# Performance work log

Hardware: AMD Instinct MI355X
Metric: run time of the kernel (lower is better)

The kernel has to match this reference:

```python
import jax, jax.numpy as jnp
import numpy as np
import math

B, T, D_MODEL, N_HEAD = 2, 2048, 1024, 16
NUM_BUCKETS, MAX_DIST = 32, 128
D_HEAD = D_MODEL // N_HEAD


def _relative_position_bucket(rel_pos, num_buckets=NUM_BUCKETS, max_distance=MAX_DIST):
    # bidirectional=True branch of the torch code
    nb = num_buckets // 2
    buckets = (rel_pos > 0).astype(jnp.int32) * nb
    rel_pos = jnp.abs(rel_pos)
    max_exact = nb // 2
    is_small = rel_pos < max_exact
    # guard log(0); masked out by is_small anyway
    large = max_exact + (
        jnp.log(jnp.maximum(rel_pos, 1).astype(jnp.float32) / max_exact)
        / math.log(max_distance / max_exact) * (nb - max_exact)
    ).astype(jnp.int32)
    large = jnp.minimum(large, nb - 1)
    return buckets + jnp.where(is_small, rel_pos, large)


def compute_bias(rel_bias, q_len, kv_len):
    qp = jnp.arange(q_len, dtype=jnp.int32)[:, None]
    kp = jnp.arange(kv_len, dtype=jnp.int32)[None, :]
    buckets = _relative_position_bucket(kp - qp)          # [Tq, Tkv]
    vals = rel_bias[buckets]                              # [Tq, Tkv, H]
    return jnp.transpose(vals, (2, 0, 1))                 # [H, Tq, Tkv]


def setup_inputs() -> dict:
    key = jax.random.key(0)
    ks = jax.random.split(key, 9)
    inp = {
        'q': jax.random.normal(ks[0], (B, T, D_MODEL), jnp.float32),
        'k': jax.random.normal(ks[1], (B, T, D_MODEL), jnp.float32),
        'v': jax.random.normal(ks[2], (B, T, D_MODEL), jnp.float32),
        'mask': jax.random.randint(ks[3], (B, T, T), 0, 2, jnp.int32),
        'Wq': jax.random.normal(ks[4], (D_MODEL, D_MODEL), jnp.float32) * 0.02,
        'Wk': jax.random.normal(ks[5], (D_MODEL, D_MODEL), jnp.float32) * 0.02,
        'Wv': jax.random.normal(ks[6], (D_MODEL, D_MODEL), jnp.float32) * 0.02,
        'Wfc': jax.random.normal(ks[7], (D_MODEL, D_MODEL), jnp.float32) * 0.02,
        'rel_bias': jax.random.normal(ks[8], (NUM_BUCKETS, N_HEAD), jnp.float32) * 0.02,
    }
    return inp


def reference(q, k, v, mask, Wq, Wk, Wv, Wfc, rel_bias):
    b, tq, _ = q.shape
    tkv = k.shape[1]
    qh = (q @ Wq).reshape(b, tq, N_HEAD, D_HEAD)
    kh = (k @ Wk).reshape(b, tkv, N_HEAD, D_HEAD)
    vh = (v @ Wv).reshape(b, tkv, N_HEAD, D_HEAD)
    attn = jnp.einsum('blhd,bthd->bhlt', qh, kh) / np.sqrt(D_HEAD).astype(np.float32)
    position_bias = compute_bias(rel_bias, tq, tkv)       # [H, Tq, Tkv]
    attn = attn + position_bias[None]                     # broadcast over batch
    attn = jnp.where(mask[:, None] == 0, -1e9, attn)
    attn = jax.nn.softmax(attn, axis=-1)                  # dropout: eval mode (identity)
    out = jnp.einsum('bhlt,bthd->blhd', attn, vh).reshape(b, tq, D_MODEL)
    out = out @ Wfc
    return out, position_bias[:, None]                    # bias returned as [H,1,Tq,Tkv] like torch
```

## Files before the change

### kernel.cpp

```cpp
#include <hip/hip_runtime.h>
#include <math.h>

#define TT 2048
#define BB 2
#define HH 16
#define DMODEL 1024
#define NREL 4095

typedef __attribute__((ext_vector_type(8)))  _Float16 half8;
typedef __attribute__((ext_vector_type(4)))  _Float16 half4;
typedef __attribute__((ext_vector_type(16))) float    f32x16;
typedef __attribute__((ext_vector_type(4)))  int      int4v;

__device__ __forceinline__ f32x16 zero16() {
    f32x16 v;
#pragma unroll
    for (int i = 0; i < 16; ++i) v[i] = 0.f;
    return v;
}

__device__ __forceinline__ unsigned pkh(float a, float b) {
    union { _Float16 h[2]; unsigned u; } x;
    x.h[0] = (_Float16)a; x.h[1] = (_Float16)b;
    return x.u;
}

__device__ __forceinline__ void gload16(const void* g, void* l) {
    __builtin_amdgcn_global_load_lds(
        (const __attribute__((address_space(1))) void*)g,
        (__attribute__((address_space(3))) void*)l, 16, 0, 0);
}

__device__ __forceinline__ int rel_bucket(int rel) {
    int base = rel > 0 ? 16 : 0;
    int r = rel < 0 ? -rel : rel;
    int lb;
    if (r < 8)       lb = r;
    else if (r < 12) lb = 8;
    else if (r < 16) lb = 9;
    else if (r < 23) lb = 10;
    else if (r < 32) lb = 11;
    else if (r < 46) lb = 12;
    else if (r < 64) lb = 13;
    else if (r < 91) lb = 14;
    else             lb = 15;
    return base + lb;
}

__global__ __launch_bounds__(256) void prep_kernel(
    const float* __restrict__ q, const float* __restrict__ k,
    const float* __restrict__ v, const int* __restrict__ mask,
    const float* __restrict__ W0, const float* __restrict__ W1,
    const float* __restrict__ W2, const float* __restrict__ W3,
    const float* __restrict__ rel_bias,
    _Float16* __restrict__ q16, _Float16* __restrict__ k16,
    _Float16* __restrict__ v16, _Float16* __restrict__ WT,
    float* __restrict__ btable, unsigned* __restrict__ mb)
{
    __shared__ float t[64][65];
    int bid = blockIdx.x, tid = threadIdx.x;
    if (bid < 256) {
        int idx = bid * 256 + tid;
        if (idx < HH * NREL) {
            int h = idx / NREL, ri = idx % NREL;
            btable[idx] = rel_bias[rel_bucket(ri - (TT - 1)) * HH + h];
        }
    } else if (bid < 1280) {
        int zz = (bid - 256) >> 8, inner = (bid - 256) & 255;
        const float* src = zz == 0 ? W0 : zz == 1 ? W1 : zz == 2 ? W2 : W3;
        _Float16* dst = WT + (size_t)zz * DMODEL * DMODEL;
        int k0 = (inner >> 4) * 64, n0 = (inner & 15) * 64;
        int r = tid >> 4, c4 = (tid & 15) * 4;
#pragma unroll
        for (int i = 0; i < 4; ++i) {
            float4 vv = *(const float4*)(src + (size_t)(k0 + r + 16 * i) * DMODEL + n0 + c4);
            t[r + 16 * i][c4] = vv.x; t[r + 16 * i][c4 + 1] = vv.y;
            t[r + 16 * i][c4 + 2] = vv.z; t[r + 16 * i][c4 + 3] = vv.w;
        }
        __syncthreads();
        int rn = tid >> 2, ck = (tid & 3) * 16;
        half8 h0, h1;
#pragma unroll
        for (int j = 0; j < 8; ++j) h0[j] = (_Float16)t[ck + j][rn];
#pragma unroll
        for (int j = 0; j < 8; ++j) h1[j] = (_Float16)t[ck + 8 + j][rn];
        *(half8*)(dst + (size_t)(n0 + rn) * DMODEL + k0 + ck) = h0;
        *(half8*)(dst + (size_t)(n0 + rn) * DMODEL + k0 + ck + 8) = h1;
    } else if (bid < 7424) {
        int zz = (bid - 1280) >> 11, inner = (bid - 1280) & 2047;
        const float* src = zz == 0 ? q : zz == 1 ? k : v;
        _Float16* dst = zz == 0 ? q16 : zz == 1 ? k16 : v16;
        int i = inner * 256 + tid;
        const float4* in4 = (const float4*)src;
        float4 v0 = in4[(size_t)i * 2], v1 = in4[(size_t)i * 2 + 1];
        half8 h = {(_Float16)v0.x, (_Float16)v0.y, (_Float16)v0.z, (_Float16)v0.w,
                   (_Float16)v1.x, (_Float16)v1.y, (_Float16)v1.z, (_Float16)v1.w};
        *(half8*)(dst + (size_t)i * 8) = h;
    } else {
        int g = (bid - 7424) * 256 + tid;
        int vv = mask[g];
        unsigned long long bal = __ballot(vv != 0);
        if ((g & 63) == 0) {
            int word = g >> 5;
            mb[word]     = (unsigned)bal;
            mb[word + 1] = (unsigned)(bal >> 32);
        }
    }
}

__global__ __launch_bounds__(256) void gemm_proj3(
    const _Float16* __restrict__ q16, const _Float16* __restrict__ k16,
    const _Float16* __restrict__ v16, const _Float16* __restrict__ WT,
    _Float16* __restrict__ qhf, _Float16* __restrict__ khf,
    _Float16* __restrict__ vtf, int zbase)
{
    __shared__ __align__(16) char lds[65536];
    int z = zbase + blockIdx.z;
    const _Float16* A  = z == 0 ? q16 : z == 1 ? k16 : v16;
    const _Float16* Bt = WT + (size_t)z * DMODEL * DMODEL;
    int bm = blockIdx.x * 128, bn = blockIdx.y * 128;
    int tid = threadIdx.x;
    int wv = tid >> 6, lane = tid & 63, hi = lane >> 5;
    int lo = lane & 31;
    int wr = wv >> 1, wc = wv & 1;
    int srow = wv * 32 + (lane >> 3);
    int scol = (lane & 7) * 8;
    const _Float16* Abase = A  + (size_t)(bm + srow) * DMODEL + scol;
    const _Float16* Bbase = Bt + (size_t)(bn + srow) * DMODEL + scol;

    f32x16 acc[2][2];
    acc[0][0] = zero16(); acc[0][1] = zero16();
    acc[1][0] = zero16(); acc[1][1] = zero16();

    auto stage = [&](int buf, int kt) {
#pragma unroll
        for (int t = 0; t < 4; ++t) {
            gload16(Abase + (size_t)t * 8 * DMODEL + kt * 64, lds + buf + wv * 4096 + t * 1024);
            gload16(Bbase + (size_t)t * 8 * DMODEL + kt * 64, lds + buf + 16384 + wv * 4096 + t * 1024);
        }
    };
    auto compute = [&](int buf) {
#pragma unroll
        for (int kk = 0; kk < 4; ++kk) {
            int cs = 2 * kk + hi;
            half8 a[2], b[2];
#pragma unroll
            for (int i = 0; i < 2; ++i) {
                a[i] = *(const half8*)(lds + buf + (wr * 64 + i * 32 + lo) * 128 + cs * 16);
                b[i] = *(const half8*)(lds + buf + 16384 + (wc * 64 + i * 32 + lo) * 128 + cs * 16);
            }
            acc[0][0] = __builtin_amdgcn_mfma_f32_32x32x16_f16(a[0], b[0], acc[0][0], 0, 0, 0);
            acc[0][1] = __builtin_amdgcn_mfma_f32_32x32x16_f16(a[0], b[1], acc[0][1], 0, 0, 0);
            acc[1][0] = __builtin_amdgcn_mfma_f32_32x32x16_f16(a[1], b[0], acc[1][0], 0, 0, 0);
            acc[1][1] = __builtin_amdgcn_mfma_f32_32x32x16_f16(a[1], b[1], acc[1][1], 0, 0, 0);
        }
    };

    stage(0, 0);
    __syncthreads();
    for (int kt = 0; kt < 16; kt += 2) {
        stage(32768, kt + 1);
        compute(0);
        __syncthreads();
        stage(0, kt + 2 < 16 ? kt + 2 : 15);
        compute(32768);
        __syncthreads();
    }

    if (z < 2) {
        _Float16* C = z == 0 ? qhf : khf;
#pragma unroll
        for (int j = 0; j < 2; ++j) {
            int n = bn + wc * 64 + j * 32 + lo;
            int h = n >> 6, d = n & 63;
#pragma unroll
            for (int i = 0; i < 2; ++i) {
                int mb2 = bm + wr * 64 + i * 32 + 4 * hi;
#pragma unroll
                for (int r = 0; r < 16; ++r) {
                    int m = mb2 + (r & 3) + 8 * (r >> 2);
                    int b = m >> 11, t = m & (TT - 1);
                    C[((size_t)(b * HH + h) * TT + t) * 64 + d] = (_Float16)acc[i][j][r];
                }
            }
        }
    } else {
#pragma unroll
        for (int j = 0; j < 2; ++j) {
            int n = bn + wc * 64 + j * 32 + lo;
            int h = n >> 6, d = n & 63;
#pragma unroll
            for (int i = 0; i < 2; ++i) {
                int mb2 = bm + wr * 64 + i * 32 + 4 * hi;
                int b = mb2 >> 11, tb = mb2 & (TT - 1);
#pragma unroll
                for (int r4 = 0; r4 < 4; ++r4) {
                    half4 hv = {(_Float16)acc[i][j][4 * r4 + 0], (_Float16)acc[i][j][4 * r4 + 1],
                                (_Float16)acc[i][j][4 * r4 + 2], (_Float16)acc[i][j][4 * r4 + 3]};
                    *(half4*)(vtf + ((size_t)(b * HH + h) * 64 + d) * TT + tb + 8 * r4) = hv;
                }
            }
        }
    }
}

template<int NSPLIT>
__global__ __launch_bounds__(256, 2) void attn_mfma(
    const _Float16* __restrict__ qh, const _Float16* __restrict__ kh,
    const _Float16* __restrict__ vt, const unsigned* __restrict__ maskbits,
    const float* __restrict__ btable, _Float16* __restrict__ Oout,
    float* __restrict__ ml)
{
    __shared__ float bias_lds[4096];
    int bid = blockIdx.x;
    int j = bid >> 3;
    int qt = j & 15;
    int sp, grp;
    if (NSPLIT == 2) { sp = (j >> 4) & 1; grp = j >> 5; }
    else             { sp = 0;            grp = j >> 4; }
    int bh = (bid & 7) + 8 * grp;
    int h = bh & 15, b = bh >> 4;
    int tid = threadIdx.x;
    int wv = tid >> 6, lane = tid & 63, lo = lane & 31, hi = lane >> 5;
    int q0 = qt * 128 + wv * 32;

    {
        const float* bsrc = btable + h * NREL;
#pragma unroll
        for (int i = 0; i < 16; ++i) {
            int idx = i * 256 + tid;
            bias_lds[idx] = bsrc[idx < NREL ? idx : NREL - 1];
        }
    }

    const size_t bhoff = (size_t)(b * HH + h);
    const _Float16* Q = qh + (bhoff * TT + q0) * 64;
    const _Float16* K = kh + bhoff * TT * 64;
    const _Float16* V = vt + bhoff * 64 * TT;

    half8 qf[4];
#pragma unroll
    for (int c = 0; c < 4; ++c)
        qf[c] = *(const half8*)(Q + (size_t)lo * 64 + c * 16 + hi * 8);

    const int bofs = (TT - 1) - (q0 + lo) + 4 * hi;
    const unsigned* mw = maskbits + ((size_t)b * TT + q0 + lo) * 64;

    f32x16 acco0 = zero16(), acco1 = zero16();
    float m = -INFINITY, l = 0.f;

    __syncthreads();

    const int ktb = sp * (32 / NSPLIT);
    for (int kt = ktb; kt < ktb + 32 / NSPLIT; ++kt) {
        int k0 = kt * 64;
        unsigned wm0 = mw[2 * kt], wm1 = mw[2 * kt + 1];

        f32x16 accs0 = zero16(), accs1 = zero16();
        {
            half8 kf[4];
#pragma unroll
            for (int c = 0; c < 4; ++c)
                kf[c] = *(const half8*)(K + (size_t)(k0 + lo) * 64 + c * 16 + hi * 8);
            __builtin_amdgcn_s_setprio(1);
#pragma unroll
            for (int c = 0; c < 4; ++c)
                accs0 = __builtin_amdgcn_mfma_f32_32x32x16_f16(kf[c], qf[c], accs0, 0, 0, 0);
            __builtin_amdgcn_s_setprio(0);
#pragma unroll
            for (int c = 0; c < 4; ++c)
                kf[c] = *(const half8*)(K + (size_t)(k0 + 32 + lo) * 64 + c * 16 + hi * 8);
            __builtin_amdgcn_s_setprio(1);
#pragma unroll
            for (int c = 0; c < 4; ++c)
                accs1 = __builtin_amdgcn_mfma_f32_32x32x16_f16(kf[c], qf[c], accs1, 0, 0, 0);
            __builtin_amdgcn_s_setprio(0);
        }

        unsigned ws0 = wm0 >> (hi * 4), ws1 = wm1 >> (hi * 4);
        int bbase = bofs + k0;
#pragma unroll
        for (int r = 0; r < 16; ++r) {
            int sh = (r & 3) + 8 * (r >> 2);
            float s0 = fmaf(accs0[r], 0.125f, bias_lds[bbase + sh]);
            float s1 = fmaf(accs1[r], 0.125f, bias_lds[bbase + sh + 32]);
            accs0[r] = ((ws0 >> sh) & 1) ? s0 : -1e9f;
            accs1[r] = ((ws1 >> sh) & 1) ? s1 : -1e9f;
        }

        float tr[8];
#pragma unroll
        for (int r = 0; r < 8; ++r)
            tr[r] = fmaxf(fmaxf(accs0[r], accs0[r + 8]), fmaxf(accs1[r], accs1[r + 8]));
#pragma unroll
        for (int r = 0; r < 4; ++r) tr[r] = fmaxf(tr[r], tr[r + 4]);
        float tm = fmaxf(fmaxf(tr[0], tr[1]), fmaxf(tr[2], tr[3]));
        tm = fmaxf(tm, __shfl_xor(tm, 32));
        float mnew = fmaxf(m, tm);
        float corr = __expf(m - mnew);
        m = mnew;

#pragma unroll
        for (int r = 0; r < 16; ++r) accs0[r] = __expf(accs0[r] - m);
#pragma unroll
        for (int r = 0; r < 16; ++r) accs1[r] = __expf(accs1[r] - m);
#pragma unroll
        for (int r = 0; r < 8; ++r)
            tr[r] = (accs0[r] + accs0[r + 8]) + (accs1[r] + accs1[r + 8]);
#pragma unroll
        for (int r = 0; r < 4; ++r) tr[r] += tr[r + 4];
        float rs = (tr[0] + tr[1]) + (tr[2] + tr[3]);
        rs += __shfl_xor(rs, 32);
        l = l * corr + rs;
#pragma unroll
        for (int r = 0; r < 16; ++r) { acco0[r] *= corr; acco1[r] *= corr; }

        half8 pb[4];
#pragma unroll
        for (int g = 0; g < 2; ++g)
#pragma unroll
            for (int hc = 0; hc < 2; ++hc) {
                int r0 = hc * 8;
                float p0 = g ? accs1[r0 + 0] : accs0[r0 + 0];
                float p1 = g ? accs1[r0 + 1] : accs0[r0 + 1];
                float p2 = g ? accs1[r0 + 2] : accs0[r0 + 2];
                float p3 = g ? accs1[r0 + 3] : accs0[r0 + 3];
                float p4 = g ? accs1[r0 + 4] : accs0[r0 + 4];
                float p5 = g ? accs1[r0 + 5] : accs0[r0 + 5];
                float p6 = g ? accs1[r0 + 6] : accs0[r0 + 6];
                float p7 = g ? accs1[r0 + 7] : accs0[r0 + 7];
                unsigned w0 = pkh(p0, p1);
                unsigned w2 = pkh(p4, p5);
                asm("v_permlane32_swap_b32 %0, %1" : "+v"(w0), "+v"(w2));
                unsigned w1 = pkh(p2, p3);
                unsigned w3 = pkh(p6, p7);
                asm("v_permlane32_swap_b32 %0, %1" : "+v"(w1), "+v"(w3));
                union { int4v i; half8 hf; } cv;
                cv.i = (int4v){(int)w0, (int)w1, (int)w2, (int)w3};
                pb[2 * g + hc] = cv.hf;
            }

        {
            half8 vf[4];
#pragma unroll
            for (int c = 0; c < 4; ++c)
                vf[c] = *(const half8*)(V + (size_t)lo * TT + k0 + c * 16 + hi * 8);
            __builtin_amdgcn_s_setprio(1);
#pragma unroll
            for (int c = 0; c < 4; ++c)
                acco0 = __builtin_amdgcn_mfma_f32_32x32x16_f16(vf[c], pb[c], acco0, 0, 0, 0);
            __builtin_amdgcn_s_setprio(0);
#pragma unroll
            for (int c = 0; c < 4; ++c)
                vf[c] = *(const half8*)(V + (size_t)(32 + lo) * TT + k0 + c * 16 + hi * 8);
            __builtin_amdgcn_s_setprio(1);
#pragma unroll
            for (int c = 0; c < 4; ++c)
                acco1 = __builtin_amdgcn_mfma_f32_32x32x16_f16(vf[c], pb[c], acco1, 0, 0, 0);
            __builtin_amdgcn_s_setprio(0);
        }
    }

    float inv = 1.f / l;
    _Float16* op = Oout + (size_t)sp * (BB * HH * TT * 64) + (bhoff * TT + q0 + lo) * 64;
#pragma unroll
    for (int r4 = 0; r4 < 4; ++r4) {
        int d0 = 8 * r4 + 4 * hi;
        half4 h0 = {(_Float16)(acco0[4 * r4 + 0] * inv), (_Float16)(acco0[4 * r4 + 1] * inv),
                    (_Float16)(acco0[4 * r4 + 2] * inv), (_Float16)(acco0[4 * r4 + 3] * inv)};
        *(half4*)(op + d0) = h0;
        half4 h1 = {(_Float16)(acco1[4 * r4 + 0] * inv), (_Float16)(acco1[4 * r4 + 1] * inv),
                    (_Float16)(acco1[4 * r4 + 2] * inv), (_Float16)(acco1[4 * r4 + 3] * inv)};
        *(half4*)(op + d0 + 32) = h1;
    }
    if (NSPLIT == 2 && hi == 0) {
        int row = (int)(bhoff * TT) + q0 + lo;
        ml[sp * 131072 + row]         = m;
        ml[sp * 131072 + 65536 + row] = l;
    }
}

__global__ __launch_bounds__(256) void combine_kernel(
    const _Float16* __restrict__ Ohalf, const float* __restrict__ ml,
    _Float16* __restrict__ O)
{
    int idx = blockIdx.x * 256 + threadIdx.x;
    int row = idx >> 3, d8 = (idx & 7) * 8;
    float m0 = ml[row],          l0 = ml[65536 + row];
    float m1 = ml[131072 + row], l1 = ml[196608 + row];
    float mm = fmaxf(m0, m1);
    float w0 = __expf(m0 - mm) * l0, w1 = __expf(m1 - mm) * l1;
    float dn = fmaxf(w0 + w1, 1e-30f);
    float c0 = w0 / dn, c1 = w1 / dn;
    half8 a = *(const half8*)(Ohalf + (size_t)row * 64 + d8);
    half8 b = *(const half8*)(Ohalf + (size_t)(BB * HH * TT * 64) + (size_t)row * 64 + d8);
    half8 o;
#pragma unroll
    for (int jj = 0; jj < 8; ++jj)
        o[jj] = (_Float16)(c0 * (float)a[jj] + c1 * (float)b[jj]);
    *(half8*)(O + (size_t)row * 64 + d8) = o;
}

__global__ __launch_bounds__(256) void fc_bias_kernel(
    const _Float16* __restrict__ O, const _Float16* __restrict__ Bt,
    float* __restrict__ out0, const float* __restrict__ btable,
    float* __restrict__ out1)
{
    __shared__ __align__(16) char lds[65536];
    int bid = blockIdx.x, tid = threadIdx.x;
    if (bid >= 256) {
        const int n4 = HH * TT * TT / 4, stride = 2048 * 256;
        for (int i4 = (bid - 256) * 256 + tid; i4 < n4; i4 += stride) {
            int i = i4 * 4;
            int kk = i & (TT - 1);
            int qq = (i >> 11) & (TT - 1);
            int hh2 = i >> 22;
            const float* btp = btable + hh2 * NREL + (kk - qq + (TT - 1));
            float4 vv = make_float4(btp[0], btp[1], btp[2], btp[3]);
            reinterpret_cast<float4*>(out1)[i4] = vv;
        }
        return;
    }
    int bm = (bid & 31) * 128, bn = (bid >> 5) * 128;
    int wv = tid >> 6, lane = tid & 63, lo = lane & 31, hi = lane >> 5;
    int wr = wv >> 1, wc = wv & 1;
    int srow = wv * 32 + (lane >> 3);
    int scol = (lane & 7) * 8;
    int bb = bm >> 11, tbase = bm & (TT - 1);
    const _Float16* Abase = O + ((size_t)(bb * HH) * TT + tbase + srow) * 64 + scol;
    const _Float16* Bbase = Bt + (size_t)(bn + srow) * DMODEL + scol;

    f32x16 acc[2][2];
    acc[0][0] = zero16(); acc[0][1] = zero16();
    acc[1][0] = zero16(); acc[1][1] = zero16();

    auto stage = [&](int buf, int kt) {
#pragma unroll
        for (int t = 0; t < 4; ++t) {
            gload16(Abase + (size_t)kt * TT * 64 + (size_t)t * 8 * 64, lds + buf + wv * 4096 + t * 1024);
            gload16(Bbase + (size_t)t * 8 * DMODEL + kt * 64, lds + buf + 16384 + wv * 4096 + t * 1024);
        }
    };
    auto compute = [&](int buf) {
#pragma unroll
        for (int kk = 0; kk < 4; ++kk) {
            int cs = 2 * kk + hi;
            half8 a[2], b[2];
#pragma unroll
            for (int i = 0; i < 2; ++i) {
                a[i] = *(const half8*)(lds + buf + (wr * 64 + i * 32 + lo) * 128 + cs * 16);
                b[i] = *(const half8*)(lds + buf + 16384 + (wc * 64 + i * 32 + lo) * 128 + cs * 16);
            }
            acc[0][0] = __builtin_amdgcn_mfma_f32_32x32x16_f16(a[0], b[0], acc[0][0], 0, 0, 0);
            acc[0][1] = __builtin_amdgcn_mfma_f32_32x32x16_f16(a[0], b[1], acc[0][1], 0, 0, 0);
            acc[1][0] = __builtin_amdgcn_mfma_f32_32x32x16_f16(a[1], b[0], acc[1][0], 0, 0, 0);
            acc[1][1] = __builtin_amdgcn_mfma_f32_32x32x16_f16(a[1], b[1], acc[1][1], 0, 0, 0);
        }
    };

    stage(0, 0);
    __syncthreads();
    for (int kt = 0; kt < 16; kt += 2) {
        stage(32768, kt + 1);
        compute(0);
        __syncthreads();
        stage(0, kt + 2 < 16 ? kt + 2 : 15);
        compute(32768);
        __syncthreads();
    }

#pragma unroll
    for (int j = 0; j < 2; ++j) {
        int n = bn + wc * 64 + j * 32 + lo;
#pragma unroll
        for (int i = 0; i < 2; ++i) {
            int mb2 = bm + wr * 64 + i * 32 + 4 * hi;
#pragma unroll
            for (int r = 0; r < 16; ++r) {
                int m = mb2 + (r & 3) + 8 * (r >> 2);
                out0[(size_t)m * DMODEL + n] = acc[i][j][r];
            }
        }
    }
}

extern "C" void kernel_launch(void* const* d_in, const int* in_sizes, int n_in,
                              void* d_out, int out_size, void* d_ws, size_t ws_size,
                              hipStream_t stream) {
    const float* q        = (const float*)d_in[0];
    const float* k        = (const float*)d_in[1];
    const float* v        = (const float*)d_in[2];
    const int*   mask     = (const int*)  d_in[3];
    const float* Wq       = (const float*)d_in[4];
    const float* Wk       = (const float*)d_in[5];
    const float* Wv       = (const float*)d_in[6];
    const float* Wfc      = (const float*)d_in[7];
    const float* rel_bias = (const float*)d_in[8];

    float* out0 = (float*)d_out;
    float* out1 = out0 + (size_t)BB * TT * DMODEL;

    char* w = (char*)d_ws;
    _Float16* q16 = (_Float16*)(w);
    _Float16* k16 = (_Float16*)(w + ((size_t)8  << 20));
    _Float16* v16 = (_Float16*)(w + ((size_t)16 << 20));
    _Float16* qhf = (_Float16*)(w + ((size_t)24 << 20));
    _Float16* khf = (_Float16*)(w + ((size_t)32 << 20));
    _Float16* WT  = (_Float16*)(w + ((size_t)40 << 20));
    float*    btable = (float*)(w + ((size_t)48 << 20));
    unsigned* mbits  = (unsigned*)(w + ((size_t)48 << 20) + ((size_t)1 << 19));
    bool big = ws_size >= ((size_t)58 << 20);
    _Float16* vtf = big ? (_Float16*)(w + ((size_t)49 << 20) + ((size_t)1 << 19))
                        : k16;
    _Float16* Ohalf = (_Float16*)w;
    float*    ml    = (float*)(w + ((size_t)40 << 20));
    _Float16* O     = v16;

    prep_kernel<<<dim3(40192), dim3(256), 0, stream>>>(
        q, k, v, mask, Wq, Wk, Wv, Wfc, rel_bias, q16, k16, v16, WT, btable, mbits);

    if (big) {
        gemm_proj3<<<dim3(32, 8, 3), dim3(256), 0, stream>>>(q16, k16, v16, WT,
                                                             qhf, khf, vtf, 0);
        attn_mfma<2><<<dim3(BB * HH * 16 * 2), dim3(256), 0, stream>>>(
            qhf, khf, vtf, mbits, btable, Ohalf, ml);
        combine_kernel<<<dim3(2048), dim3(256), 0, stream>>>(Ohalf, ml, O);
    } else {
        gemm_proj3<<<dim3(32, 8, 1), dim3(256), 0, stream>>>(q16, k16, v16, WT, qhf, khf, vtf, 0);
        gemm_proj3<<<dim3(32, 8, 1), dim3(256), 0, stream>>>(q16, k16, v16, WT, qhf, khf, vtf, 1);
        gemm_proj3<<<dim3(32, 8, 1), dim3(256), 0, stream>>>(q16, k16, v16, WT, qhf, khf, vtf, 2);
        attn_mfma<1><<<dim3(BB * HH * 16), dim3(256), 0, stream>>>(
            qhf, khf, vtf, mbits, btable, O, ml);
    }

    fc_bias_kernel<<<dim3(2304), dim3(256), 0, stream>>>(
        O, WT + (size_t)3 * DMODEL * DMODEL, out0, btable, out1);
}
```

Baseline: 293.6 us.

## Drop split-KV attention, process 128-key tiles, and use exp2 softmax

```diff
diff --git a/kernel.cpp b/kernel.cpp
--- a/kernel.cpp
+++ b/kernel.cpp
@@ -11,6 +11,8 @@
 typedef __attribute__((ext_vector_type(4)))  _Float16 half4;
 typedef __attribute__((ext_vector_type(16))) float    f32x16;
 typedef __attribute__((ext_vector_type(4)))  int      int4v;
+
+#define EXP2F(x) __builtin_amdgcn_exp2f(x)
 
 __device__ __forceinline__ f32x16 zero16() {
     f32x16 v;
@@ -204,21 +206,15 @@
     }
 }
 
-template<int NSPLIT>
-__global__ __launch_bounds__(256, 2) void attn_mfma(
+__global__ __launch_bounds__(256) void attn_mfma(
     const _Float16* __restrict__ qh, const _Float16* __restrict__ kh,
     const _Float16* __restrict__ vt, const unsigned* __restrict__ maskbits,
-    const float* __restrict__ btable, _Float16* __restrict__ Oout,
-    float* __restrict__ ml)
+    const float* __restrict__ btable, _Float16* __restrict__ Oout)
 {
     __shared__ float bias_lds[4096];
     int bid = blockIdx.x;
-    int j = bid >> 3;
-    int qt = j & 15;
-    int sp, grp;
-    if (NSPLIT == 2) { sp = (j >> 4) & 1; grp = j >> 5; }
-    else             { sp = 0;            grp = j >> 4; }
-    int bh = (bid & 7) + 8 * grp;
+    int xcd = bid & 7, j = bid >> 3;
+    int qt = j & 15, bh = xcd + 8 * (j >> 4);
     int h = bh & 15, b = bh >> 4;
     int tid = threadIdx.x;
     int wv = tid >> 6, lane = tid & 63, lo = lane & 31, hi = lane >> 5;
@@ -229,7 +225,7 @@
 #pragma unroll
         for (int i = 0; i < 16; ++i) {
             int idx = i * 256 + tid;
-            bias_lds[idx] = bsrc[idx < NREL ? idx : NREL - 1];
+            bias_lds[idx] = bsrc[idx < NREL ? idx : NREL - 1] * 1.44269504f;
         }
     }
 
@@ -245,18 +241,19 @@
 
     const int bofs = (TT - 1) - (q0 + lo) + 4 * hi;
     const unsigned* mw = maskbits + ((size_t)b * TT + q0 + lo) * 64;
+    const float SC = 0.125f * 1.44269504f;
 
     f32x16 acco0 = zero16(), acco1 = zero16();
     float m = -INFINITY, l = 0.f;
 
     __syncthreads();
 
-    const int ktb = sp * (32 / NSPLIT);
-    for (int kt = ktb; kt < ktb + 32 / NSPLIT; ++kt) {
-        int k0 = kt * 64;
-        unsigned wm0 = mw[2 * kt], wm1 = mw[2 * kt + 1];
-
-        f32x16 accs0 = zero16(), accs1 = zero16();
+    for (int kt = 0; kt < 16; ++kt) {
+        int k0 = kt * 128;
+        unsigned wmA0 = mw[4 * kt], wmA1 = mw[4 * kt + 1];
+        unsigned wmB0 = mw[4 * kt + 2], wmB1 = mw[4 * kt + 3];
+
+        f32x16 sA0 = zero16(), sA1 = zero16(), sB0 = zero16(), sB1 = zero16();
         {
             half8 kf[4];
 #pragma unroll
@@ -265,7 +262,7 @@
             __builtin_amdgcn_s_setprio(1);
 #pragma unroll
             for (int c = 0; c < 4; ++c)
-                accs0 = __builtin_amdgcn_mfma_f32_32x32x16_f16(kf[c], qf[c], accs0, 0, 0, 0);
+                sA0 = __builtin_amdgcn_mfma_f32_32x32x16_f16(kf[c], qf[c], sA0, 0, 0, 0);
             __builtin_amdgcn_s_setprio(0);
 #pragma unroll
             for (int c = 0; c < 4; ++c)
@@ -273,40 +270,69 @@
             __builtin_amdgcn_s_setprio(1);
 #pragma unroll
             for (int c = 0; c < 4; ++c)
-                accs1 = __builtin_amdgcn_mfma_f32_32x32x16_f16(kf[c], qf[c], accs1, 0, 0, 0);
-            __builtin_amdgcn_s_setprio(0);
-        }
-
-        unsigned ws0 = wm0 >> (hi * 4), ws1 = wm1 >> (hi * 4);
+                sA1 = __builtin_amdgcn_mfma_f32_32x32x16_f16(kf[c], qf[c], sA1, 0, 0, 0);
+            __builtin_amdgcn_s_setprio(0);
+#pragma unroll
+            for (int c = 0; c < 4; ++c)
+                kf[c] = *(const half8*)(K + (size_t)(k0 + 64 + lo) * 64 + c * 16 + hi * 8);
+            __builtin_amdgcn_s_setprio(1);
+#pragma unroll
+            for (int c = 0; c < 4; ++c)
+                sB0 = __builtin_amdgcn_mfma_f32_32x32x16_f16(kf[c], qf[c], sB0, 0, 0, 0);
+            __builtin_amdgcn_s_setprio(0);
+#pragma unroll
+            for (int c = 0; c < 4; ++c)
+                kf[c] = *(const half8*)(K + (size_t)(k0 + 96 + lo) * 64 + c * 16 + hi * 8);
+            __builtin_amdgcn_s_setprio(1);
+#pragma unroll
+            for (int c = 0; c < 4; ++c)
+                sB1 = __builtin_amdgcn_mfma_f32_32x32x16_f16(kf[c], qf[c], sB1, 0, 0, 0);
+            __builtin_amdgcn_s_setprio(0);
+        }
+
+        unsigned wsA0 = wmA0 >> (hi * 4), wsA1 = wmA1 >> (hi * 4);
+        unsigned wsB0 = wmB0 >> (hi * 4), wsB1 = wmB1 >> (hi * 4);
         int bbase = bofs + k0;
 #pragma unroll
         for (int r = 0; r < 16; ++r) {
             int sh = (r & 3) + 8 * (r >> 2);
-            float s0 = fmaf(accs0[r], 0.125f, bias_lds[bbase + sh]);
-            float s1 = fmaf(accs1[r], 0.125f, bias_lds[bbase + sh + 32]);
-            accs0[r] = ((ws0 >> sh) & 1) ? s0 : -1e9f;
-            accs1[r] = ((ws1 >> sh) & 1) ? s1 : -1e9f;
+            float a0 = fmaf(sA0[r], SC, bias_lds[bbase + sh]);
+            float a1 = fmaf(sA1[r], SC, bias_lds[bbase + sh + 32]);
+            float b0 = fmaf(sB0[r], SC, bias_lds[bbase + sh + 64]);
+            float b1 = fmaf(sB1[r], SC, bias_lds[bbase + sh + 96]);
+            sA0[r] = ((wsA0 >> sh) & 1) ? a0 : -1e9f;
+            sA1[r] = ((wsA1 >> sh) & 1) ? a1 : -1e9f;
+            sB0[r] = ((wsB0 >> sh) & 1) ? b0 : -1e9f;
+            sB1[r] = ((wsB1 >> sh) & 1) ? b1 : -1e9f;
         }
 
         float tr[8];
 #pragma unroll
-        for (int r = 0; r < 8; ++r)
-            tr[r] = fmaxf(fmaxf(accs0[r], accs0[r + 8]), fmaxf(accs1[r], accs1[r + 8]));
+        for (int r = 0; r < 8; ++r) {
+            float x0 = fmaxf(fmaxf(sA0[r], sA0[r + 8]), fmaxf(sA1[r], sA1[r + 8]));
+            float x1 = fmaxf(fmaxf(sB0[r], sB0[r + 8]), fmaxf(sB1[r], sB1[r + 8]));
+            tr[r] = fmaxf(x0, x1);
+        }
 #pragma unroll
         for (int r = 0; r < 4; ++r) tr[r] = fmaxf(tr[r], tr[r + 4]);
         float tm = fmaxf(fmaxf(tr[0], tr[1]), fmaxf(tr[2], tr[3]));
         tm = fmaxf(tm, __shfl_xor(tm, 32));
         float mnew = fmaxf(m, tm);
-        float corr = __expf(m - mnew);
+        float corr = EXP2F(m - mnew);
         m = mnew;
 
 #pragma unroll
-        for (int r = 0; r < 16; ++r) accs0[r] = __expf(accs0[r] - m);
-#pragma unroll
-        for (int r = 0; r < 16; ++r) accs1[r] = __expf(accs1[r] - m);
+        for (int r = 0; r < 16; ++r) sA0[r] = EXP2F(sA0[r] - m);
+#pragma unroll
+        for (int r = 0; r < 16; ++r) sA1[r] = EXP2F(sA1[r] - m);
+#pragma unroll
+        for (int r = 0; r < 16; ++r) sB0[r] = EXP2F(sB0[r] - m);
+#pragma unroll
+        for (int r = 0; r < 16; ++r) sB1[r] = EXP2F(sB1[r] - m);
 #pragma unroll
         for (int r = 0; r < 8; ++r)
-            tr[r] = (accs0[r] + accs0[r + 8]) + (accs1[r] + accs1[r + 8]);
+            tr[r] = ((sA0[r] + sA0[r + 8]) + (sA1[r] + sA1[r + 8]))
+                  + ((sB0[r] + sB0[r + 8]) + (sB1[r] + sB1[r + 8]));
 #pragma unroll
         for (int r = 0; r < 4; ++r) tr[r] += tr[r + 4];
         float rs = (tr[0] + tr[1]) + (tr[2] + tr[3]);
@@ -315,20 +341,20 @@
 #pragma unroll
         for (int r = 0; r < 16; ++r) { acco0[r] *= corr; acco1[r] *= corr; }
 
-        half8 pb[4];
+        half8 pbA[4], pbB[4];
 #pragma unroll
         for (int g = 0; g < 2; ++g)
 #pragma unroll
             for (int hc = 0; hc < 2; ++hc) {
                 int r0 = hc * 8;
-                float p0 = g ? accs1[r0 + 0] : accs0[r0 + 0];
-                float p1 = g ? accs1[r0 + 1] : accs0[r0 + 1];
-                float p2 = g ? accs1[r0 + 2] : accs0[r0 + 2];
-                float p3 = g ? accs1[r0 + 3] : accs0[r0 + 3];
-                float p4 = g ? accs1[r0 + 4] : accs0[r0 + 4];
-                float p5 = g ? accs1[r0 + 5] : accs0[r0 + 5];
-                float p6 = g ? accs1[r0 + 6] : accs0[r0 + 6];
-                float p7 = g ? accs1[r0 + 7] : accs0[r0 + 7];
+                float p0 = g ? sA1[r0 + 0] : sA0[r0 + 0];
+                float p1 = g ? sA1[r0 + 1] : sA0[r0 + 1];
+                float p2 = g ? sA1[r0 + 2] : sA0[r0 + 2];
+                float p3 = g ? sA1[r0 + 3] : sA0[r0 + 3];
+                float p4 = g ? sA1[r0 + 4] : sA0[r0 + 4];
+                float p5 = g ? sA1[r0 + 5] : sA0[r0 + 5];
+                float p6 = g ? sA1[r0 + 6] : sA0[r0 + 6];
+                float p7 = g ? sA1[r0 + 7] : sA0[r0 + 7];
                 unsigned w0 = pkh(p0, p1);
                 unsigned w2 = pkh(p4, p5);
                 asm("v_permlane32_swap_b32 %0, %1" : "+v"(w0), "+v"(w2));
@@ -337,7 +363,30 @@
                 asm("v_permlane32_swap_b32 %0, %1" : "+v"(w1), "+v"(w3));
                 union { int4v i; half8 hf; } cv;
                 cv.i = (int4v){(int)w0, (int)w1, (int)w2, (int)w3};
-                pb[2 * g + hc] = cv.hf;
+                pbA[2 * g + hc] = cv.hf;
+            }
+#pragma unroll
+        for (int g = 0; g < 2; ++g)
+#pragma unroll
+            for (int hc = 0; hc < 2; ++hc) {
+                int r0 = hc * 8;
+                float p0 = g ? sB1[r0 + 0] : sB0[r0 + 0];
+                float p1 = g ? sB1[r0 + 1] : sB0[r0 + 1];
+                float p2 = g ? sB1[r0 + 2] : sB0[r0 + 2];
+                float p3 = g ? sB1[r0 + 3] : sB0[r0 + 3];
+                float p4 = g ? sB1[r0 + 4] : sB0[r0 + 4];
+                float p5 = g ? sB1[r0 + 5] : sB0[r0 + 5];
+                float p6 = g ? sB1[r0 + 6] : sB0[r0 + 6];
+                float p7 = g ? sB1[r0 + 7] : sB0[r0 + 7];
+                unsigned w0 = pkh(p0, p1);
+                unsigned w2 = pkh(p4, p5);
+                asm("v_permlane32_swap_b32 %0, %1" : "+v"(w0), "+v"(w2));
+                unsigned w1 = pkh(p2, p3);
+                unsigned w3 = pkh(p6, p7);
+                asm("v_permlane32_swap_b32 %0, %1" : "+v"(w1), "+v"(w3));
+                union { int4v i; half8 hf; } cv;
+                cv.i = (int4v){(int)w0, (int)w1, (int)w2, (int)w3};
+                pbB[2 * g + hc] = cv.hf;
             }
 
         {
@@ -348,7 +397,15 @@
             __builtin_amdgcn_s_setprio(1);
 #pragma unroll
             for (int c = 0; c < 4; ++c)
-                acco0 = __builtin_amdgcn_mfma_f32_32x32x16_f16(vf[c], pb[c], acco0, 0, 0, 0);
+                acco0 = __builtin_amdgcn_mfma_f32_32x32x16_f16(vf[c], pbA[c], acco0, 0, 0, 0);
+            __builtin_amdgcn_s_setprio(0);
+#pragma unroll
+            for (int c = 0; c < 4; ++c)
+                vf[c] = *(const half8*)(V + (size_t)lo * TT + k0 + 64 + c * 16 + hi * 8);
+            __builtin_amdgcn_s_setprio(1);
+#pragma unroll
+            for (int c = 0; c < 4; ++c)
+                acco0 = __builtin_amdgcn_mfma_f32_32x32x16_f16(vf[c], pbB[c], acco0, 0, 0, 0);
             __builtin_amdgcn_s_setprio(0);
 #pragma unroll
             for (int c = 0; c < 4; ++c)
@@ -356,13 +413,21 @@
             __builtin_amdgcn_s_setprio(1);
 #pragma unroll
             for (int c = 0; c < 4; ++c)
-                acco1 = __builtin_amdgcn_mfma_f32_32x32x16_f16(vf[c], pb[c], acco1, 0, 0, 0);
+                acco1 = __builtin_amdgcn_mfma_f32_32x32x16_f16(vf[c], pbA[c], acco1, 0, 0, 0);
+            __builtin_amdgcn_s_setprio(0);
+#pragma unroll
+            for (int c = 0; c < 4; ++c)
+                vf[c] = *(const half8*)(V + (size_t)(32 + lo) * TT + k0 + 64 + c * 16 + hi * 8);
+            __builtin_amdgcn_s_setprio(1);
+#pragma unroll
+            for (int c = 0; c < 4; ++c)
+                acco1 = __builtin_amdgcn_mfma_f32_32x32x16_f16(vf[c], pbB[c], acco1, 0, 0, 0);
             __builtin_amdgcn_s_setprio(0);
         }
     }
 
     float inv = 1.f / l;
-    _Float16* op = Oout + (size_t)sp * (BB * HH * TT * 64) + (bhoff * TT + q0 + lo) * 64;
+    _Float16* op = Oout + (bhoff * TT + q0 + lo) * 64;
 #pragma unroll
     for (int r4 = 0; r4 < 4; ++r4) {
         int d0 = 8 * r4 + 4 * hi;
@@ -373,32 +438,6 @@
                     (_Float16)(acco1[4 * r4 + 2] * inv), (_Float16)(acco1[4 * r4 + 3] * inv)};
         *(half4*)(op + d0 + 32) = h1;
     }
-    if (NSPLIT == 2 && hi == 0) {
-        int row = (int)(bhoff * TT) + q0 + lo;
-        ml[sp * 131072 + row]         = m;
-        ml[sp * 131072 + 65536 + row] = l;
-    }
-}
-
-__global__ __launch_bounds__(256) void combine_kernel(
-    const _Float16* __restrict__ Ohalf, const float* __restrict__ ml,
-    _Float16* __restrict__ O)
-{
-    int idx = blockIdx.x * 256 + threadIdx.x;
-    int row = idx >> 3, d8 = (idx & 7) * 8;
-    float m0 = ml[row],          l0 = ml[65536 + row];
-    float m1 = ml[131072 + row], l1 = ml[196608 + row];
-    float mm = fmaxf(m0, m1);
-    float w0 = __expf(m0 - mm) * l0, w1 = __expf(m1 - mm) * l1;
-    float dn = fmaxf(w0 + w1, 1e-30f);
-    float c0 = w0 / dn, c1 = w1 / dn;
-    half8 a = *(const half8*)(Ohalf + (size_t)row * 64 + d8);
-    half8 b = *(const half8*)(Ohalf + (size_t)(BB * HH * TT * 64) + (size_t)row * 64 + d8);
-    half8 o;
-#pragma unroll
-    for (int jj = 0; jj < 8; ++jj)
-        o[jj] = (_Float16)(c0 * (float)a[jj] + c1 * (float)b[jj]);
-    *(half8*)(O + (size_t)row * 64 + d8) = o;
 }
 
 __global__ __launch_bounds__(256) void fc_bias_kernel(
@@ -512,9 +551,7 @@
     bool big = ws_size >= ((size_t)58 << 20);
     _Float16* vtf = big ? (_Float16*)(w + ((size_t)49 << 20) + ((size_t)1 << 19))
                         : k16;
-    _Float16* Ohalf = (_Float16*)w;
-    float*    ml    = (float*)(w + ((size_t)40 << 20));
-    _Float16* O     = v16;
+    _Float16* O = v16;
 
     prep_kernel<<<dim3(40192), dim3(256), 0, stream>>>(
         q, k, v, mask, Wq, Wk, Wv, Wfc, rel_bias, q16, k16, v16, WT, btable, mbits);
@@ -522,16 +559,14 @@
     if (big) {
         gemm_proj3<<<dim3(32, 8, 3), dim3(256), 0, stream>>>(q16, k16, v16, WT,
                                                              qhf, khf, vtf, 0);
-        attn_mfma<2><<<dim3(BB * HH * 16 * 2), dim3(256), 0, stream>>>(
-            qhf, khf, vtf, mbits, btable, Ohalf, ml);
-        combine_kernel<<<dim3(2048), dim3(256), 0, stream>>>(Ohalf, ml, O);
     } else {
         gemm_proj3<<<dim3(32, 8, 1), dim3(256), 0, stream>>>(q16, k16, v16, WT, qhf, khf, vtf, 0);
         gemm_proj3<<<dim3(32, 8, 1), dim3(256), 0, stream>>>(q16, k16, v16, WT, qhf, khf, vtf, 1);
         gemm_proj3<<<dim3(32, 8, 1), dim3(256), 0, stream>>>(q16, k16, v16, WT, qhf, khf, vtf, 2);
-        attn_mfma<1><<<dim3(BB * HH * 16), dim3(256), 0, stream>>>(
-            qhf, khf, vtf, mbits, btable, O, ml);
-    }
+    }
+
+    attn_mfma<<<dim3(BB * HH * 16), dim3(256), 0, stream>>>(
+        qhf, khf, vtf, mbits, btable, O);
 
     fc_bias_kernel<<<dim3(2304), dim3(256), 0, stream>>>(
         O, WT + (size_t)3 * DMODEL * DMODEL, out0, btable, out1);
```

Result: faster. 281.3 us, median of 2 (-4.2%).

## Drop split-KV attention, software-pipeline QK^T of next tile with exp2 softmax

Applied to the files above, without the earlier changes.

```diff
diff --git a/kernel.cpp b/kernel.cpp
--- a/kernel.cpp
+++ b/kernel.cpp
@@ -11,6 +11,8 @@
 typedef __attribute__((ext_vector_type(4)))  _Float16 half4;
 typedef __attribute__((ext_vector_type(16))) float    f32x16;
 typedef __attribute__((ext_vector_type(4)))  int      int4v;
+
+#define EXP2F(x) __builtin_amdgcn_exp2f(x)
 
 __device__ __forceinline__ f32x16 zero16() {
     f32x16 v;
@@ -204,21 +206,15 @@
     }
 }
 
-template<int NSPLIT>
-__global__ __launch_bounds__(256, 2) void attn_mfma(
+__global__ __launch_bounds__(256) void attn_mfma(
     const _Float16* __restrict__ qh, const _Float16* __restrict__ kh,
     const _Float16* __restrict__ vt, const unsigned* __restrict__ maskbits,
-    const float* __restrict__ btable, _Float16* __restrict__ Oout,
-    float* __restrict__ ml)
+    const float* __restrict__ btable, _Float16* __restrict__ Oout)
 {
     __shared__ float bias_lds[4096];
     int bid = blockIdx.x;
-    int j = bid >> 3;
-    int qt = j & 15;
-    int sp, grp;
-    if (NSPLIT == 2) { sp = (j >> 4) & 1; grp = j >> 5; }
-    else             { sp = 0;            grp = j >> 4; }
-    int bh = (bid & 7) + 8 * grp;
+    int xcd = bid & 7, j = bid >> 3;
+    int qt = j & 15, bh = xcd + 8 * (j >> 4);
     int h = bh & 15, b = bh >> 4;
     int tid = threadIdx.x;
     int wv = tid >> 6, lane = tid & 63, lo = lane & 31, hi = lane >> 5;
@@ -229,7 +225,7 @@
 #pragma unroll
         for (int i = 0; i < 16; ++i) {
             int idx = i * 256 + tid;
-            bias_lds[idx] = bsrc[idx < NREL ? idx : NREL - 1];
+            bias_lds[idx] = bsrc[idx < NREL ? idx : NREL - 1] * 1.44269504f;
         }
     }
 
@@ -245,68 +241,77 @@
 
     const int bofs = (TT - 1) - (q0 + lo) + 4 * hi;
     const unsigned* mw = maskbits + ((size_t)b * TT + q0 + lo) * 64;
+    const float SC = 0.125f * 1.44269504f;
 
     f32x16 acco0 = zero16(), acco1 = zero16();
     float m = -INFINITY, l = 0.f;
 
     __syncthreads();
 
-    const int ktb = sp * (32 / NSPLIT);
-    for (int kt = ktb; kt < ktb + 32 / NSPLIT; ++kt) {
+    f32x16 sE0 = zero16(), sE1 = zero16();
+    f32x16 sO0 = zero16(), sO1 = zero16();
+    {
+        half8 kf[4];
+#pragma unroll
+        for (int c = 0; c < 4; ++c)
+            kf[c] = *(const half8*)(K + (size_t)lo * 64 + c * 16 + hi * 8);
+#pragma unroll
+        for (int c = 0; c < 4; ++c)
+            sE0 = __builtin_amdgcn_mfma_f32_32x32x16_f16(kf[c], qf[c], sE0, 0, 0, 0);
+#pragma unroll
+        for (int c = 0; c < 4; ++c)
+            kf[c] = *(const half8*)(K + (size_t)(32 + lo) * 64 + c * 16 + hi * 8);
+#pragma unroll
+        for (int c = 0; c < 4; ++c)
+            sE1 = __builtin_amdgcn_mfma_f32_32x32x16_f16(kf[c], qf[c], sE1, 0, 0, 0);
+    }
+
+    auto body = [&](int kt, f32x16& c0, f32x16& c1, f32x16& n0, f32x16& n1) {
         int k0 = kt * 64;
+        int kn = (kt < 31 ? kt + 1 : kt) * 64;
+        half8 kfA[4], kfB[4], vfA[4], vfB[4];
+#pragma unroll
+        for (int c = 0; c < 4; ++c)
+            kfA[c] = *(const half8*)(K + (size_t)(kn + lo) * 64 + c * 16 + hi * 8);
+#pragma unroll
+        for (int c = 0; c < 4; ++c)
+            kfB[c] = *(const half8*)(K + (size_t)(kn + 32 + lo) * 64 + c * 16 + hi * 8);
+#pragma unroll
+        for (int c = 0; c < 4; ++c)
+            vfA[c] = *(const half8*)(V + (size_t)lo * TT + k0 + c * 16 + hi * 8);
+#pragma unroll
+        for (int c = 0; c < 4; ++c)
+            vfB[c] = *(const half8*)(V + (size_t)(32 + lo) * TT + k0 + c * 16 + hi * 8);
         unsigned wm0 = mw[2 * kt], wm1 = mw[2 * kt + 1];
-
-        f32x16 accs0 = zero16(), accs1 = zero16();
-        {
-            half8 kf[4];
-#pragma unroll
-            for (int c = 0; c < 4; ++c)
-                kf[c] = *(const half8*)(K + (size_t)(k0 + lo) * 64 + c * 16 + hi * 8);
-            __builtin_amdgcn_s_setprio(1);
-#pragma unroll
-            for (int c = 0; c < 4; ++c)
-                accs0 = __builtin_amdgcn_mfma_f32_32x32x16_f16(kf[c], qf[c], accs0, 0, 0, 0);
-            __builtin_amdgcn_s_setprio(0);
-#pragma unroll
-            for (int c = 0; c < 4; ++c)
-                kf[c] = *(const half8*)(K + (size_t)(k0 + 32 + lo) * 64 + c * 16 + hi * 8);
-            __builtin_amdgcn_s_setprio(1);
-#pragma unroll
-            for (int c = 0; c < 4; ++c)
-                accs1 = __builtin_amdgcn_mfma_f32_32x32x16_f16(kf[c], qf[c], accs1, 0, 0, 0);
-            __builtin_amdgcn_s_setprio(0);
-        }
 
         unsigned ws0 = wm0 >> (hi * 4), ws1 = wm1 >> (hi * 4);
         int bbase = bofs + k0;
 #pragma unroll
         for (int r = 0; r < 16; ++r) {
             int sh = (r & 3) + 8 * (r >> 2);
-            float s0 = fmaf(accs0[r], 0.125f, bias_lds[bbase + sh]);
-            float s1 = fmaf(accs1[r], 0.125f, bias_lds[bbase + sh + 32]);
-            accs0[r] = ((ws0 >> sh) & 1) ? s0 : -1e9f;
-            accs1[r] = ((ws1 >> sh) & 1) ? s1 : -1e9f;
-        }
-
+            float a0 = fmaf(c0[r], SC, bias_lds[bbase + sh]);
+            float a1 = fmaf(c1[r], SC, bias_lds[bbase + sh + 32]);
+            c0[r] = ((ws0 >> sh) & 1) ? a0 : -1e9f;
+            c1[r] = ((ws1 >> sh) & 1) ? a1 : -1e9f;
+        }
         float tr[8];
 #pragma unroll
         for (int r = 0; r < 8; ++r)
-            tr[r] = fmaxf(fmaxf(accs0[r], accs0[r + 8]), fmaxf(accs1[r], accs1[r + 8]));
+            tr[r] = fmaxf(fmaxf(c0[r], c0[r + 8]), fmaxf(c1[r], c1[r + 8]));
 #pragma unroll
         for (int r = 0; r < 4; ++r) tr[r] = fmaxf(tr[r], tr[r + 4]);
         float tm = fmaxf(fmaxf(tr[0], tr[1]), fmaxf(tr[2], tr[3]));
         tm = fmaxf(tm, __shfl_xor(tm, 32));
         float mnew = fmaxf(m, tm);
-        float corr = __expf(m - mnew);
+        float corr = EXP2F(m - mnew);
         m = mnew;
-
-#pragma unroll
-        for (int r = 0; r < 16; ++r) accs0[r] = __expf(accs0[r] - m);
-#pragma unroll
-        for (int r = 0; r < 16; ++r) accs1[r] = __expf(accs1[r] - m);
+#pragma unroll
+        for (int r = 0; r < 16; ++r) c0[r] = EXP2F(c0[r] - m);
+#pragma unroll
+        for (int r = 0; r < 16; ++r) c1[r] = EXP2F(c1[r] - m);
 #pragma unroll
         for (int r = 0; r < 8; ++r)
-            tr[r] = (accs0[r] + accs0[r + 8]) + (accs1[r] + accs1[r + 8]);
+            tr[r] = (c0[r] + c0[r + 8]) + (c1[r] + c1[r + 8]);
 #pragma unroll
         for (int r = 0; r < 4; ++r) tr[r] += tr[r + 4];
         float rs = (tr[0] + tr[1]) + (tr[2] + tr[3]);
@@ -321,14 +326,14 @@
 #pragma unroll
             for (int hc = 0; hc < 2; ++hc) {
                 int r0 = hc * 8;
-                float p0 = g ? accs1[r0 + 0] : accs0[r0 + 0];
-                float p1 = g ? accs1[r0 + 1] : accs0[r0 + 1];
-                float p2 = g ? accs1[r0 + 2] : accs0[r0 + 2];
-                float p3 = g ? accs1[r0 + 3] : accs0[r0 + 3];
-                float p4 = g ? accs1[r0 + 4] : accs0[r0 + 4];
-                float p5 = g ? accs1[r0 + 5] : accs0[r0 + 5];
-                float p6 = g ? accs1[r0 + 6] : accs0[r0 + 6];
-                float p7 = g ? accs1[r0 + 7] : accs0[r0 + 7];
+                float p0 = g ? c1[r0 + 0] : c0[r0 + 0];
+                float p1 = g ? c1[r0 + 1] : c0[r0 + 1];
+                float p2 = g ? c1[r0 + 2] : c0[r0 + 2];
+                float p3 = g ? c1[r0 + 3] : c0[r0 + 3];
+                float p4 = g ? c1[r0 + 4] : c0[r0 + 4];
+                float p5 = g ? c1[r0 + 5] : c0[r0 + 5];
+                float p6 = g ? c1[r0 + 6] : c0[r0 + 6];
+                float p7 = g ? c1[r0 + 7] : c0[r0 + 7];
                 unsigned w0 = pkh(p0, p1);
                 unsigned w2 = pkh(p4, p5);
                 asm("v_permlane32_swap_b32 %0, %1" : "+v"(w0), "+v"(w2));
@@ -340,29 +345,34 @@
                 pb[2 * g + hc] = cv.hf;
             }
 
-        {
-            half8 vf[4];
-#pragma unroll
-            for (int c = 0; c < 4; ++c)
-                vf[c] = *(const half8*)(V + (size_t)lo * TT + k0 + c * 16 + hi * 8);
-            __builtin_amdgcn_s_setprio(1);
-#pragma unroll
-            for (int c = 0; c < 4; ++c)
-                acco0 = __builtin_amdgcn_mfma_f32_32x32x16_f16(vf[c], pb[c], acco0, 0, 0, 0);
-            __builtin_amdgcn_s_setprio(0);
-#pragma unroll
-            for (int c = 0; c < 4; ++c)
-                vf[c] = *(const half8*)(V + (size_t)(32 + lo) * TT + k0 + c * 16 + hi * 8);
-            __builtin_amdgcn_s_setprio(1);
-#pragma unroll
-            for (int c = 0; c < 4; ++c)
-                acco1 = __builtin_amdgcn_mfma_f32_32x32x16_f16(vf[c], pb[c], acco1, 0, 0, 0);
-            __builtin_amdgcn_s_setprio(0);
-        }
+        __builtin_amdgcn_s_setprio(1);
+#pragma unroll
+        for (int c = 0; c < 4; ++c)
+            acco0 = __builtin_amdgcn_mfma_f32_32x32x16_f16(vfA[c], pb[c], acco0, 0, 0, 0);
+#pragma unroll
+        for (int c = 0; c < 4; ++c)
+            acco1 = __builtin_amdgcn_mfma_f32_32x32x16_f16(vfB[c], pb[c], acco1, 0, 0, 0);
+        __builtin_amdgcn_s_setprio(0);
+
+        n0 = zero16(); n1 = zero16();
+        __builtin_amdgcn_s_setprio(1);
+#pragma unroll
+        for (int c = 0; c < 4; ++c)
+            n0 = __builtin_amdgcn_mfma_f32_32x32x16_f16(kfA[c], qf[c], n0, 0, 0, 0);
+#pragma unroll
+        for (int c = 0; c < 4; ++c)
+            n1 = __builtin_amdgcn_mfma_f32_32x32x16_f16(kfB[c], qf[c], n1, 0, 0, 0);
+        __builtin_amdgcn_s_setprio(0);
+    };
+
+#pragma unroll 1
+    for (int kt = 0; kt < 32; kt += 2) {
+        body(kt,     sE0, sE1, sO0, sO1);
+        body(kt + 1, sO0, sO1, sE0, sE1);
     }
 
     float inv = 1.f / l;
-    _Float16* op = Oout + (size_t)sp * (BB * HH * TT * 64) + (bhoff * TT + q0 + lo) * 64;
+    _Float16* op = Oout + (bhoff * TT + q0 + lo) * 64;
 #pragma unroll
     for (int r4 = 0; r4 < 4; ++r4) {
         int d0 = 8 * r4 + 4 * hi;
@@ -373,32 +383,6 @@
                     (_Float16)(acco1[4 * r4 + 2] * inv), (_Float16)(acco1[4 * r4 + 3] * inv)};
         *(half4*)(op + d0 + 32) = h1;
     }
-    if (NSPLIT == 2 && hi == 0) {
-        int row = (int)(bhoff * TT) + q0 + lo;
-        ml[sp * 131072 + row]         = m;
-        ml[sp * 131072 + 65536 + row] = l;
-    }
-}
-
-__global__ __launch_bounds__(256) void combine_kernel(
-    const _Float16* __restrict__ Ohalf, const float* __restrict__ ml,
-    _Float16* __restrict__ O)
-{
-    int idx = blockIdx.x * 256 + threadIdx.x;
-    int row = idx >> 3, d8 = (idx & 7) * 8;
-    float m0 = ml[row],          l0 = ml[65536 + row];
-    float m1 = ml[131072 + row], l1 = ml[196608 + row];
-    float mm = fmaxf(m0, m1);
-    float w0 = __expf(m0 - mm) * l0, w1 = __expf(m1 - mm) * l1;
-    float dn = fmaxf(w0 + w1, 1e-30f);
-    float c0 = w0 / dn, c1 = w1 / dn;
-    half8 a = *(const half8*)(Ohalf + (size_t)row * 64 + d8);
-    half8 b = *(const half8*)(Ohalf + (size_t)(BB * HH * TT * 64) + (size_t)row * 64 + d8);
-    half8 o;
-#pragma unroll
-    for (int jj = 0; jj < 8; ++jj)
-        o[jj] = (_Float16)(c0 * (float)a[jj] + c1 * (float)b[jj]);
-    *(half8*)(O + (size_t)row * 64 + d8) = o;
 }
 
 __global__ __launch_bounds__(256) void fc_bias_kernel(
@@ -512,9 +496,7 @@
     bool big = ws_size >= ((size_t)58 << 20);
     _Float16* vtf = big ? (_Float16*)(w + ((size_t)49 << 20) + ((size_t)1 << 19))
                         : k16;
-    _Float16* Ohalf = (_Float16*)w;
-    float*    ml    = (float*)(w + ((size_t)40 << 20));
-    _Float16* O     = v16;
+    _Float16* O = v16;
 
     prep_kernel<<<dim3(40192), dim3(256), 0, stream>>>(
         q, k, v, mask, Wq, Wk, Wv, Wfc, rel_bias, q16, k16, v16, WT, btable, mbits);
@@ -522,16 +504,14 @@
     if (big) {
         gemm_proj3<<<dim3(32, 8, 3), dim3(256), 0, stream>>>(q16, k16, v16, WT,
                                                              qhf, khf, vtf, 0);
-        attn_mfma<2><<<dim3(BB * HH * 16 * 2), dim3(256), 0, stream>>>(
-            qhf, khf, vtf, mbits, btable, Ohalf, ml);
-        combine_kernel<<<dim3(2048), dim3(256), 0, stream>>>(Ohalf, ml, O);
     } else {
         gemm_proj3<<<dim3(32, 8, 1), dim3(256), 0, stream>>>(q16, k16, v16, WT, qhf, khf, vtf, 0);
         gemm_proj3<<<dim3(32, 8, 1), dim3(256), 0, stream>>>(q16, k16, v16, WT, qhf, khf, vtf, 1);
         gemm_proj3<<<dim3(32, 8, 1), dim3(256), 0, stream>>>(q16, k16, v16, WT, qhf, khf, vtf, 2);
-        attn_mfma<1><<<dim3(BB * HH * 16), dim3(256), 0, stream>>>(
-            qhf, khf, vtf, mbits, btable, O, ml);
-    }
+    }
+
+    attn_mfma<<<dim3(BB * HH * 16), dim3(256), 0, stream>>>(
+        qhf, khf, vtf, mbits, btable, O);
 
     fc_bias_kernel<<<dim3(2304), dim3(256), 0, stream>>>(
         O, WT + (size_t)3 * DMODEL * DMODEL, out0, btable, out1);
```

New measurement: 284.4 us. 3.1% less time.
